# Kernel tuning notes

Hardware: AMD Instinct MI355X
Metric: run time of the kernel (lower is better)

## Reference

```python
import jax, jax.numpy as jnp
import numpy as np

B, H, L, D = 2, 16, 2048, 128

def setup_inputs() -> dict:
    key = jax.random.key(0)
    kq, kk, kv = jax.random.split(key, 3)
    Q = jax.random.normal(kq, (B, H, L, D), dtype=jnp.float32)
    K = jax.random.normal(kk, (B, H, L, D), dtype=jnp.float32)
    V = jax.random.normal(kv, (B, H, L, D), dtype=jnp.float32)
    # causal mask: True where attention is allowed
    mask = jnp.broadcast_to(jnp.tril(jnp.ones((L, L), dtype=bool)), (B, H, L, L))
    return {"Q": Q, "K": K, "V": V, "mask": mask}

def reference(Q, K, V, mask):
    d_k = Q.shape[-1]
    scale = 1.0 / jnp.sqrt(jnp.asarray(d_k, dtype=Q.dtype))
    # [B,H,Lq,Lk] score matrix (naive materialization, as in the original)
    scores = jnp.einsum('bhqd,bhkd->bhqk', Q, K) * scale
    scores = jnp.where(mask, scores, -jnp.inf)
    attn = jax.nn.softmax(scores, axis=-1)
    return jnp.einsum('bhqk,bhkd->bhqd', attn, V)
```

## Files before the change

kernel.cpp:

```cpp
#include <hip/hip_runtime.h>
#include <hip/hip_bf16.h>

namespace {

constexpr int Bc = 2, Hc = 16, Lc = 2048, Dc = 128;
constexpr int KVBLK = 64;
constexpr int BH  = Bc * Hc;
constexpr int NKT = Lc / KVBLK;
constexpr int QB  = 128;
constexpr int NQT = Lc / QB;
constexpr float SCALE = 0.08838834764831845f * 1.4426950408889634f;

using f32x4   = __attribute__((ext_vector_type(4))) float;
using f32x16  = __attribute__((ext_vector_type(16))) float;
using short8  = __attribute__((ext_vector_type(8))) short;

union FragU { short8 v; short4 h[2]; };
union PFU  { short8 v; unsigned u[4]; };

__device__ inline short f2bf(float f) {
  unsigned u = __builtin_bit_cast(unsigned, f);
  u += 0x7fffu + ((u >> 16) & 1u);
  return (short)(u >> 16);
}

__device__ inline void gload_lds16(const short* g, short* l) {
  __builtin_amdgcn_global_load_lds(
      (const __attribute__((address_space(1))) void*)g,
      (__attribute__((address_space(3))) void*)l, 16, 0, 0);
}

__global__ __launch_bounds__(256) void conv_kv(const float* __restrict__ Kg,
                                               const float* __restrict__ Vg,
                                               short* __restrict__ Kw,
                                               short* __restrict__ Vw) {
  __shared__ short Vs[64 * 130];
  const int b = blockIdx.x;
  if (b < 4096) {
    int tid = b * 256 + threadIdx.x;
    int x   = tid & 15;
    int row = (tid >> 4) & 63;
    int tb  = tid >> 10;
    int g   = x ^ (row & 7);
    int chunk = g >> 1, hi = g & 1;
    const float* src = Kg + ((size_t)tb * 64 + row) * 128 + chunk * 16 + hi * 4;
    float4 a = *(const float4*)src;
    float4 c = *(const float4*)(src + 8);
    short8 v;
    v[0] = f2bf(a.x); v[1] = f2bf(a.y); v[2] = f2bf(a.z); v[3] = f2bf(a.w);
    v[4] = f2bf(c.x); v[5] = f2bf(c.y); v[6] = f2bf(c.z); v[7] = f2bf(c.w);
    *(short8*)(Kw + (size_t)tb * 8192 + row * 128 + x * 8) = v;
  } else {
    int tb  = b - 4096;
    int tid = threadIdx.x;
    const float* vt = Vg + (size_t)tb * 8192;
#pragma unroll
    for (int p = 0; p < 8; ++p) {
      int g  = p * 256 + tid;
      int kv = g >> 5;
      int c4 = g & 31;
      float4 v = *((const float4*)vt + g);
      short* d = &Vs[kv * 130 + c4 * 4];
      d[0] = f2bf(v.x); d[1] = f2bf(v.y); d[2] = f2bf(v.z); d[3] = f2bf(v.w);
    }
    __syncthreads();
#pragma unroll
    for (int p = 0; p < 4; ++p) {
      int gg = p * 256 + tid;
      int d  = gg >> 3;
      int x  = gg & 7;
      int g  = x ^ (d & 7);
      int chunk = g >> 1, hi = g & 1;
      int k0 = chunk * 16 + hi * 4;
      short8 o;
#pragma unroll
      for (int j = 0; j < 4; ++j) o[j]     = Vs[(k0 + j)     * 130 + d];
#pragma unroll
      for (int j = 0; j < 4; ++j) o[4 + j] = Vs[(k0 + 8 + j) * 130 + d];
      *(short8*)(Vw + (size_t)tb * 8192 + d * 64 + x * 8) = o;
    }
  }
}

__global__ __launch_bounds__(256, 2) void attn_fwd5(
    const float* __restrict__ Qg, const short* __restrict__ Kw,
    const short* __restrict__ Vw, float* __restrict__ Og) {

  __shared__ __align__(16) short K2[2][8192];
  __shared__ __align__(16) short V3[3][8192];

  const int tid  = threadIdx.x;
  const int wave = tid >> 6;
  const int lane = tid & 63;
  const int hi   = lane >> 5;
  const int ln   = lane & 31;
  const int sw   = (ln & 7) << 4;

  const int bid = blockIdx.x;
  const int bh  = bid & (BH - 1);
  const int r5  = bid >> 5;
  const int qt  = (bid < 256) ? (NQT - 1 - r5) : (r5 - 8);
  const int q0w = qt * QB + wave * 32;

  const float* Qp  = Qg + (size_t)bh * Lc * Dc;
  float*       Op  = Og + (size_t)bh * Lc * Dc;
  const short* Kwp = Kw + (size_t)bh * NKT * 8192;
  const short* Vwp = Vw + (size_t)bh * NKT * 8192;

  short8 qf[8];
  {
    const float* qrow = Qp + (size_t)(q0w + ln) * Dc + hi * 4;
#pragma unroll
    for (int ks = 0; ks < 8; ++ks) {
      float4 a = *(const float4*)(qrow + ks * 16);
      float4 b = *(const float4*)(qrow + ks * 16 + 8);
      short8 v;
      v[0] = f2bf(a.x * SCALE); v[1] = f2bf(a.y * SCALE);
      v[2] = f2bf(a.z * SCALE); v[3] = f2bf(a.w * SCALE);
      v[4] = f2bf(b.x * SCALE); v[5] = f2bf(b.y * SCALE);
      v[6] = f2bf(b.z * SCALE); v[7] = f2bf(b.w * SCALE);
      qf[ks] = v;
    }
  }

  float m_run = -1e30f, l_run = 0.0f;
  f32x16 oacc[4];
#pragma unroll
  for (int nt = 0; nt < 4; ++nt)
#pragma unroll
    for (int r = 0; r < 16; ++r) oacc[nt][r] = 0.0f;

  const int ntiles = 2 * (qt + 1);
  const int tlast  = min(ntiles - 1, (q0w + 31) >> 6);

  auto stage = [&](int t, int kb, int vb) {
    const short* gk = Kwp + (size_t)t * 8192 + tid * 8;
    const short* gv = Vwp + (size_t)t * 8192 + tid * 8;
    short* lk = &K2[kb][tid * 8];
    short* lv = &V3[vb][tid * 8];
#pragma unroll
    for (int i = 0; i < 4; ++i) gload_lds16(gk + i * 2048, lk + i * 2048);
#pragma unroll
    for (int i = 0; i < 4; ++i) gload_lds16(gv + i * 2048, lv + i * 2048);
  };

  stage(0, 0, 0);
  int vb_prev = 2, vb_cur = 0, vb_next = 1;
  PFU pf[4];

  for (int t = 0; t < ntiles; ++t) {
    const int cur = t & 1;
    __builtin_amdgcn_s_barrier();
    if (t + 1 < ntiles) {
      stage(t + 1, cur ^ 1, vb_next);
      asm volatile("s_waitcnt vmcnt(8)" ::: "memory");
    } else {
      asm volatile("s_waitcnt vmcnt(0)" ::: "memory");
    }
    __builtin_amdgcn_s_barrier();
    __builtin_amdgcn_sched_barrier(0);

    const bool do_t = (t <= tlast);
    const bool do_pv = (t >= 1) && (t - 1 <= tlast);
    const int kv0 = t * KVBLK;

    f32x16 s0, s1;
    if (do_t) {
      const char* Kl = (const char*)&K2[cur][0];
#pragma unroll
      for (int r = 0; r < 16; ++r) { s0[r] = 0.0f; s1[r] = 0.0f; }
      __builtin_amdgcn_s_setprio(1);
#pragma unroll
      for (int ks = 0; ks < 8; ++ks) {
        FragU a0, a1;
        int col = (ks * 32 + hi * 16) ^ sw;
        a0.v = *(const short8*)(Kl + ln * 256        + col);
        a1.v = *(const short8*)(Kl + (32 + ln) * 256 + col);
        s0 = __builtin_amdgcn_mfma_f32_32x32x16_bf16(a0.v, qf[ks], s0, 0, 0, 0);
        s1 = __builtin_amdgcn_mfma_f32_32x32x16_bf16(a1.v, qf[ks], s1, 0, 0, 0);
      }
      __builtin_amdgcn_s_setprio(0);
    }

    if (do_pv) {
      const char* Vl = (const char*)&V3[vb_prev][0];
      __builtin_amdgcn_s_setprio(1);
#pragma unroll
      for (int nt = 0; nt < 4; ++nt) {
        const char* vrow = Vl + (nt * 32 + ln) * 128;
#pragma unroll
        for (int kc = 0; kc < 4; ++kc) {
          FragU b;
          b.v = *(const short8*)(vrow + ((kc * 32 + hi * 16) ^ sw));
          oacc[nt] = __builtin_amdgcn_mfma_f32_32x32x16_bf16(pf[kc].v, b.v, oacc[nt], 0, 0, 0);
        }
      }
      __builtin_amdgcn_s_setprio(0);
    }

    if (do_t) {
      if (kv0 + 63 > q0w) {
        const int qg = q0w + ln;
#pragma unroll
        for (int r = 0; r < 16; ++r) {
          int kvr = kv0 + (r & 3) + 8 * (r >> 2) + 4 * hi;
          if (kvr > qg)      s0[r] = -1e30f;
          if (kvr + 32 > qg) s1[r] = -1e30f;
        }
      }
      float ma = s0[0], mb = s0[8], mc = s1[0], md = s1[8];
#pragma unroll
      for (int r = 1; r < 8; ++r) {
        ma = fmaxf(ma, s0[r]); mb = fmaxf(mb, s0[8 + r]);
        mc = fmaxf(mc, s1[r]); md = fmaxf(md, s1[8 + r]);
      }
      float mx = fmaxf(fmaxf(ma, mb), fmaxf(mc, md));
      mx = fmaxf(mx, __shfl_xor(mx, 32));

      if (!__all(mx - m_run <= 8.0f)) {
        float mnew = fmaxf(m_run, mx);
        float corr = exp2f(m_run - mnew);
        m_run = mnew;
        l_run *= corr;
#pragma unroll
        for (int r = 0; r < 16; ++r) {
          int qrow = (r & 3) + 8 * (r >> 2) + 4 * hi;
          float c = __shfl(corr, qrow);
#pragma unroll
          for (int nt = 0; nt < 4; ++nt) oacc[nt][r] *= c;
        }
      }

      float rsp[4] = {0.f, 0.f, 0.f, 0.f};
#pragma unroll
      for (int kc = 0; kc < 4; ++kc) {
#pragma unroll
        for (int w = 0; w < 4; ++w) {
          int e = kc * 8 + w * 2;
          float v0 = (kc < 2) ? (float)s0[e]     : (float)s1[e - 16];
          float v1 = (kc < 2) ? (float)s0[e + 1] : (float)s1[e - 15];
          float e0 = exp2f(v0 - m_run);
          float e1 = exp2f(v1 - m_run);
          rsp[w] += e0 + e1;
          asm("v_cvt_pk_bf16_f32 %0, %1, %2" : "=v"(pf[kc].u[w]) : "v"(e0), "v"(e1));
        }
      }
      float rs = (rsp[0] + rsp[1]) + (rsp[2] + rsp[3]);
      rs += __shfl_xor(rs, 32);
      l_run += rs;
    }

    int tmp = vb_prev; vb_prev = vb_cur; vb_cur = vb_next; vb_next = tmp;
  }

  if (tlast == ntiles - 1) {
    const char* Vl = (const char*)&V3[vb_prev][0];
#pragma unroll
    for (int nt = 0; nt < 4; ++nt) {
      const char* vrow = Vl + (nt * 32 + ln) * 128;
#pragma unroll
      for (int kc = 0; kc < 4; ++kc) {
        FragU b;
        b.v = *(const short8*)(vrow + ((kc * 32 + hi * 16) ^ sw));
        oacc[nt] = __builtin_amdgcn_mfma_f32_32x32x16_bf16(pf[kc].v, b.v, oacc[nt], 0, 0, 0);
      }
    }
  }

  float linv = 1.0f / l_run;
#pragma unroll
  for (int r = 0; r < 16; ++r) {
    int qrow = (r & 3) + 8 * (r >> 2) + 4 * hi;
    float il = __shfl(linv, qrow);
    float* orow = Op + (size_t)(q0w + qrow) * Dc + ln;
#pragma unroll
    for (int nt = 0; nt < 4; ++nt)
      orow[nt * 32] = oacc[nt][r] * il;
  }
}

__device__ inline unsigned packbf(float a, float b) {
  return (unsigned)(unsigned short)f2bf(a) | ((unsigned)(unsigned short)f2bf(b) << 16);
}

__global__ __launch_bounds__(256, 2) void attn_fb(
    const float* __restrict__ Qg, const float* __restrict__ Kg,
    const float* __restrict__ Vg, float* __restrict__ Og) {
  __shared__ __align__(16) short Klds[KVBLK * Dc];
  __shared__ __align__(16) short Vt[Dc * 68];
  const int tid = threadIdx.x, wave = tid >> 6, lane = tid & 63;
  const int lg = lane >> 4, lr = lane & 15;
  const int bid = blockIdx.x;
  const int bh = bid & (BH - 1);
  const int qt = 31 - (bid >> 5);
  const int q0w = qt * 64 + wave * 16;
  const float* Qp = Qg + (size_t)bh * Lc * Dc;
  const float* Kp = Kg + (size_t)bh * Lc * Dc;
  const float* Vp = Vg + (size_t)bh * Lc * Dc;
  float* Op = Og + (size_t)bh * Lc * Dc;
  short8 qf[4];
  {
    const float* qrow = Qp + (size_t)(q0w + lr) * Dc;
#pragma unroll
    for (int dc = 0; dc < 4; ++dc) {
      float4 a = *(const float4*)(qrow + dc * 32 + lg * 4);
      float4 b = *(const float4*)(qrow + dc * 32 + 16 + lg * 4);
      short8 v;
      v[0]=f2bf(a.x*SCALE); v[1]=f2bf(a.y*SCALE); v[2]=f2bf(a.z*SCALE); v[3]=f2bf(a.w*SCALE);
      v[4]=f2bf(b.x*SCALE); v[5]=f2bf(b.y*SCALE); v[6]=f2bf(b.z*SCALE); v[7]=f2bf(b.w*SCALE);
      qf[dc] = v;
    }
  }
  const f32x4 zero4 = {0.f,0.f,0.f,0.f};
  float m_run = -1e30f, l_run = 0.0f;
  f32x4 oacc[8];
#pragma unroll
  for (int dt = 0; dt < 8; ++dt) oacc[dt] = zero4;
  const int ntiles = qt + 1, c4 = tid & 31, rK = tid >> 5;
  for (int t = 0; t < ntiles; ++t) {
    const int kv0 = t * KVBLK;
    __syncthreads();
#pragma unroll
    for (int p = 0; p < 8; ++p) {
      int row = rK + p * 8;
      float4 k4 = *(const float4*)(Kp + (size_t)(kv0 + row) * Dc + c4 * 4);
      short4 pk; pk.x=f2bf(k4.x); pk.y=f2bf(k4.y); pk.z=f2bf(k4.z); pk.w=f2bf(k4.w);
      *(short4*)((char*)Klds + row * 256 + ((c4 * 8) ^ ((row & 7) << 4))) = pk;
    }
#pragma unroll
    for (int p = 0; p < 4; ++p) {
      int r0 = rK * 2 + p * 16;
      float4 v0 = *(const float4*)(Vp + (size_t)(kv0 + r0) * Dc + c4 * 4);
      float4 v1 = *(const float4*)(Vp + (size_t)(kv0 + r0 + 1) * Dc + c4 * 4);
      char* vb = (char*)Vt + r0 * 2;
      *(unsigned*)(vb + (c4*4+0)*136) = packbf(v0.x, v1.x);
      *(unsigned*)(vb + (c4*4+1)*136) = packbf(v0.y, v1.y);
      *(unsigned*)(vb + (c4*4+2)*136) = packbf(v0.z, v1.z);
      *(unsigned*)(vb + (c4*4+3)*136) = packbf(v0.w, v1.w);
    }
    __syncthreads();
    f32x4 st[4];
#pragma unroll
    for (int mt = 0; mt < 4; ++mt) st[mt] = zero4;
#pragma unroll
    for (int dc = 0; dc < 4; ++dc)
#pragma unroll
      for (int mt = 0; mt < 4; ++mt) {
        int row = mt * 16 + lr, sw2 = (row & 7) << 4;
        FragU a;
        a.h[0] = *(short4*)((char*)Klds + row*256 + ((dc*64      + lg*8) ^ sw2));
        a.h[1] = *(short4*)((char*)Klds + row*256 + ((dc*64 + 32 + lg*8) ^ sw2));
        st[mt] = __builtin_amdgcn_mfma_f32_16x16x32_bf16(a.v, qf[dc], st[mt], 0, 0, 0);
      }
    if (t == ntiles - 1) {
      const int qg = q0w + lr;
#pragma unroll
      for (int mt = 0; mt < 4; ++mt)
#pragma unroll
        for (int r = 0; r < 4; ++r)
          if (kv0 + mt * 16 + lg * 4 + r > qg) st[mt][r] = -1e30f;
    }
    float mx = st[0][0];
#pragma unroll
    for (int mt = 0; mt < 4; ++mt)
#pragma unroll
      for (int r = 0; r < 4; ++r) mx = fmaxf(mx, st[mt][r]);
    mx = fmaxf(mx, __shfl_xor(mx, 16));
    mx = fmaxf(mx, __shfl_xor(mx, 32));
    float mnew = fmaxf(m_run, mx);
    float corr = exp2f(m_run - mnew);
    m_run = mnew;
    float pr[4][4]; float rs = 0.0f;
#pragma unroll
    for (int mt = 0; mt < 4; ++mt)
#pragma unroll
      for (int r = 0; r < 4; ++r) { float e = exp2f(st[mt][r] - mnew); pr[mt][r] = e; rs += e; }
    rs += __shfl_xor(rs, 16);
    rs += __shfl_xor(rs, 32);
    l_run = l_run * corr + rs;
#pragma unroll
    for (int r = 0; r < 4; ++r) {
      float c = __shfl(corr, (lane & 48) + lg * 4 + r);
#pragma unroll
      for (int dt = 0; dt < 8; ++dt) oacc[dt][r] *= c;
    }
    short8 pf2[2];
#pragma unroll
    for (int c = 0; c < 2; ++c) {
      short8 v;
      v[0]=f2bf(pr[2*c][0]); v[1]=f2bf(pr[2*c][1]); v[2]=f2bf(pr[2*c][2]); v[3]=f2bf(pr[2*c][3]);
      v[4]=f2bf(pr[2*c+1][0]); v[5]=f2bf(pr[2*c+1][1]); v[6]=f2bf(pr[2*c+1][2]); v[7]=f2bf(pr[2*c+1][3]);
      pf2[c] = v;
    }
#pragma unroll
    for (int dt = 0; dt < 8; ++dt) {
      int rowb = (dt * 16 + lr) * 136;
#pragma unroll
      for (int c = 0; c < 2; ++c) {
        FragU b;
        b.h[0] = *(short4*)((char*)Vt + rowb + c*64      + lg*8);
        b.h[1] = *(short4*)((char*)Vt + rowb + c*64 + 32 + lg*8);
        oacc[dt] = __builtin_amdgcn_mfma_f32_16x16x32_bf16(pf2[c], b.v, oacc[dt], 0, 0, 0);
      }
    }
  }
#pragma unroll
  for (int r = 0; r < 4; ++r) {
    float li = __shfl(l_run, (lane & 48) + lg * 4 + r);
    float inv = 1.0f / li;
    float* orow = Op + (size_t)(q0w + lg * 4 + r) * Dc;
#pragma unroll
    for (int dt = 0; dt < 8; ++dt) orow[dt * 16 + lr] = oacc[dt][r] * inv;
  }
}

}

extern "C" void kernel_launch(void* const* d_in, const int* in_sizes, int n_in,
                              void* d_out, int out_size, void* d_ws, size_t ws_size,
                              hipStream_t stream) {
  const float* Q = (const float*)d_in[0];
  const float* K = (const float*)d_in[1];
  const float* V = (const float*)d_in[2];
  float* O = (float*)d_out;
  const size_t elems = (size_t)BH * Lc * Dc;
  const size_t need  = 2 * elems * sizeof(short);
  if (ws_size >= need) {
    short* Kw = (short*)d_ws;
    short* Vw = Kw + elems;
    conv_kv<<<dim3(4096 + 1024), dim3(256), 0, stream>>>(K, V, Kw, Vw);
    attn_fwd5<<<dim3(BH * NQT), dim3(256), 0, stream>>>(Q, Kw, Vw, O);
  } else {
    attn_fb<<<dim3(BH * NKT), dim3(256), 0, stream>>>(Q, K, V, O);
  }
}
```

Baseline: 95.11 us.

## Load K/V MFMA fragments directly from global into registers, drop LDS staging

The K/V pre-conversion kernel now writes bf16 data in exact per-lane MFMA fragment order, so the attention kernel can load K and V fragments straight from global memory into registers instead of staging tiles through double/triple-buffered LDS with barriers. The main loop is restructured to compute QK^T, softmax and PV within the same iteration, prefetching the next tile's fragments into registers. This removes LDS traffic and block-wide barriers, and each wave now iterates only over its own causal range. In exchange, every wave independently reads the full K/V tiles from global/L2, with no sharing across the 4 waves. The 32 extra fragment registers also raise register pressure, and the cross-iteration software pipelining of PV behind the next QK is lost.

```diff
diff --git a/kernel.cpp b/kernel.cpp
--- a/kernel.cpp
+++ b/kernel.cpp
@@ -16,18 +16,11 @@
 using short8  = __attribute__((ext_vector_type(8))) short;
 
 union FragU { short8 v; short4 h[2]; };
-union PFU  { short8 v; unsigned u[4]; };
 
 __device__ inline short f2bf(float f) {
   unsigned u = __builtin_bit_cast(unsigned, f);
   u += 0x7fffu + ((u >> 16) & 1u);
   return (short)(u >> 16);
-}
-
-__device__ inline void gload_lds16(const short* g, short* l) {
-  __builtin_amdgcn_global_load_lds(
-      (const __attribute__((address_space(1))) void*)g,
-      (__attribute__((address_space(3))) void*)l, 16, 0, 0);
 }
 
 __global__ __launch_bounds__(256) void conv_kv(const float* __restrict__ Kg,
@@ -37,19 +30,20 @@
   __shared__ short Vs[64 * 130];
   const int b = blockIdx.x;
   if (b < 4096) {
-    int tid = b * 256 + threadIdx.x;
-    int x   = tid & 15;
-    int row = (tid >> 4) & 63;
-    int tb  = tid >> 10;
-    int g   = x ^ (row & 7);
-    int chunk = g >> 1, hi = g & 1;
-    const float* src = Kg + ((size_t)tb * 64 + row) * 128 + chunk * 16 + hi * 4;
+    int tid  = b * 256 + threadIdx.x;
+    int rem  = tid & 1023;
+    int tb   = tid >> 10;
+    int ks   = rem >> 7;
+    int s    = (rem >> 6) & 1;
+    int lane = rem & 63;
+    int hi   = lane >> 5, ln = lane & 31;
+    const float* src = Kg + ((size_t)tb * 64 + s * 32 + ln) * 128 + ks * 16 + hi * 4;
     float4 a = *(const float4*)src;
     float4 c = *(const float4*)(src + 8);
     short8 v;
     v[0] = f2bf(a.x); v[1] = f2bf(a.y); v[2] = f2bf(a.z); v[3] = f2bf(a.w);
     v[4] = f2bf(c.x); v[5] = f2bf(c.y); v[6] = f2bf(c.z); v[7] = f2bf(c.w);
-    *(short8*)(Kw + (size_t)tb * 8192 + row * 128 + x * 8) = v;
+    *(short8*)(Kw + (size_t)tb * 8192 + rem * 8) = v;
   } else {
     int tb  = b - 4096;
     int tid = threadIdx.x;
@@ -66,35 +60,32 @@
     __syncthreads();
 #pragma unroll
     for (int p = 0; p < 4; ++p) {
-      int gg = p * 256 + tid;
-      int d  = gg >> 3;
-      int x  = gg & 7;
-      int g  = x ^ (d & 7);
-      int chunk = g >> 1, hi = g & 1;
-      int k0 = chunk * 16 + hi * 4;
+      int g    = p * 256 + tid;
+      int nt   = g >> 8;
+      int kc   = (g >> 6) & 3;
+      int lane = g & 63;
+      int hi   = lane >> 5, ln = lane & 31;
+      int d    = nt * 32 + ln;
+      int k0   = kc * 16 + hi * 4;
       short8 o;
 #pragma unroll
       for (int j = 0; j < 4; ++j) o[j]     = Vs[(k0 + j)     * 130 + d];
 #pragma unroll
       for (int j = 0; j < 4; ++j) o[4 + j] = Vs[(k0 + 8 + j) * 130 + d];
-      *(short8*)(Vw + (size_t)tb * 8192 + d * 64 + x * 8) = o;
-    }
-  }
-}
-
-__global__ __launch_bounds__(256, 2) void attn_fwd5(
+      *(short8*)(Vw + (size_t)tb * 8192 + g * 8) = o;
+    }
+  }
+}
+
+__global__ __launch_bounds__(256, 2) void attn_fwd6(
     const float* __restrict__ Qg, const short* __restrict__ Kw,
     const short* __restrict__ Vw, float* __restrict__ Og) {
-
-  __shared__ __align__(16) short K2[2][8192];
-  __shared__ __align__(16) short V3[3][8192];
 
   const int tid  = threadIdx.x;
   const int wave = tid >> 6;
   const int lane = tid & 63;
   const int hi   = lane >> 5;
   const int ln   = lane & 31;
-  const int sw   = (ln & 7) << 4;
 
   const int bid = blockIdx.x;
   const int bh  = bid & (BH - 1);
@@ -104,8 +95,8 @@
 
   const float* Qp  = Qg + (size_t)bh * Lc * Dc;
   float*       Op  = Og + (size_t)bh * Lc * Dc;
-  const short* Kwp = Kw + (size_t)bh * NKT * 8192;
-  const short* Vwp = Vw + (size_t)bh * NKT * 8192;
+  const short* kb  = Kw + (size_t)bh * NKT * 8192 + lane * 8;
+  const short* vb  = Vw + (size_t)bh * NKT * 8192 + lane * 8;
 
   short8 qf[8];
   {
@@ -130,140 +121,99 @@
 #pragma unroll
     for (int r = 0; r < 16; ++r) oacc[nt][r] = 0.0f;
 
-  const int ntiles = 2 * (qt + 1);
-  const int tlast  = min(ntiles - 1, (q0w + 31) >> 6);
-
-  auto stage = [&](int t, int kb, int vb) {
-    const short* gk = Kwp + (size_t)t * 8192 + tid * 8;
-    const short* gv = Vwp + (size_t)t * 8192 + tid * 8;
-    short* lk = &K2[kb][tid * 8];
-    short* lv = &V3[vb][tid * 8];
-#pragma unroll
-    for (int i = 0; i < 4; ++i) gload_lds16(gk + i * 2048, lk + i * 2048);
-#pragma unroll
-    for (int i = 0; i < 4; ++i) gload_lds16(gv + i * 2048, lv + i * 2048);
-  };
-
-  stage(0, 0, 0);
-  int vb_prev = 2, vb_cur = 0, vb_next = 1;
-  PFU pf[4];
-
-  for (int t = 0; t < ntiles; ++t) {
-    const int cur = t & 1;
-    __builtin_amdgcn_s_barrier();
-    if (t + 1 < ntiles) {
-      stage(t + 1, cur ^ 1, vb_next);
-      asm volatile("s_waitcnt vmcnt(8)" ::: "memory");
-    } else {
-      asm volatile("s_waitcnt vmcnt(0)" ::: "memory");
-    }
-    __builtin_amdgcn_s_barrier();
-    __builtin_amdgcn_sched_barrier(0);
-
-    const bool do_t = (t <= tlast);
-    const bool do_pv = (t >= 1) && (t - 1 <= tlast);
+  const int tl = (q0w + 31) >> 6;
+
+  FragU kf[16], vf[16];
+#pragma unroll
+  for (int i = 0; i < 16; ++i) kf[i].v = *(const short8*)(kb + i * 512);
+#pragma unroll
+  for (int i = 0; i < 16; ++i) vf[i].v = *(const short8*)(vb + i * 512);
+
+  for (int t = 0; t <= tl; ++t) {
+    f32x16 s0, s1;
+#pragma unroll
+    for (int r = 0; r < 16; ++r) { s0[r] = 0.0f; s1[r] = 0.0f; }
+    __builtin_amdgcn_s_setprio(1);
+#pragma unroll
+    for (int ks = 0; ks < 8; ++ks) {
+      s0 = __builtin_amdgcn_mfma_f32_32x32x16_bf16(kf[ks * 2 + 0].v, qf[ks], s0, 0, 0, 0);
+      s1 = __builtin_amdgcn_mfma_f32_32x32x16_bf16(kf[ks * 2 + 1].v, qf[ks], s1, 0, 0, 0);
+    }
+    __builtin_amdgcn_s_setprio(0);
+
+    if (t < tl) {
+      const short* kn = kb + (size_t)(t + 1) * 8192;
+#pragma unroll
+      for (int i = 0; i < 16; ++i) kf[i].v = *(const short8*)(kn + i * 512);
+    }
+
     const int kv0 = t * KVBLK;
-
-    f32x16 s0, s1;
-    if (do_t) {
-      const char* Kl = (const char*)&K2[cur][0];
-#pragma unroll
-      for (int r = 0; r < 16; ++r) { s0[r] = 0.0f; s1[r] = 0.0f; }
-      __builtin_amdgcn_s_setprio(1);
-#pragma unroll
-      for (int ks = 0; ks < 8; ++ks) {
-        FragU a0, a1;
-        int col = (ks * 32 + hi * 16) ^ sw;
-        a0.v = *(const short8*)(Kl + ln * 256        + col);
-        a1.v = *(const short8*)(Kl + (32 + ln) * 256 + col);
-        s0 = __builtin_amdgcn_mfma_f32_32x32x16_bf16(a0.v, qf[ks], s0, 0, 0, 0);
-        s1 = __builtin_amdgcn_mfma_f32_32x32x16_bf16(a1.v, qf[ks], s1, 0, 0, 0);
-      }
-      __builtin_amdgcn_s_setprio(0);
-    }
-
-    if (do_pv) {
-      const char* Vl = (const char*)&V3[vb_prev][0];
-      __builtin_amdgcn_s_setprio(1);
-#pragma unroll
-      for (int nt = 0; nt < 4; ++nt) {
-        const char* vrow = Vl + (nt * 32 + ln) * 128;
-#pragma unroll
-        for (int kc = 0; kc < 4; ++kc) {
-          FragU b;
-          b.v = *(const short8*)(vrow + ((kc * 32 + hi * 16) ^ sw));
-          oacc[nt] = __builtin_amdgcn_mfma_f32_32x32x16_bf16(pf[kc].v, b.v, oacc[nt], 0, 0, 0);
-        }
-      }
-      __builtin_amdgcn_s_setprio(0);
-    }
-
-    if (do_t) {
-      if (kv0 + 63 > q0w) {
-        const int qg = q0w + ln;
-#pragma unroll
-        for (int r = 0; r < 16; ++r) {
-          int kvr = kv0 + (r & 3) + 8 * (r >> 2) + 4 * hi;
-          if (kvr > qg)      s0[r] = -1e30f;
-          if (kvr + 32 > qg) s1[r] = -1e30f;
-        }
-      }
-      float ma = s0[0], mb = s0[8], mc = s1[0], md = s1[8];
-#pragma unroll
-      for (int r = 1; r < 8; ++r) {
-        ma = fmaxf(ma, s0[r]); mb = fmaxf(mb, s0[8 + r]);
-        mc = fmaxf(mc, s1[r]); md = fmaxf(md, s1[8 + r]);
-      }
-      float mx = fmaxf(fmaxf(ma, mb), fmaxf(mc, md));
-      mx = fmaxf(mx, __shfl_xor(mx, 32));
-
-      if (!__all(mx - m_run <= 8.0f)) {
-        float mnew = fmaxf(m_run, mx);
-        float corr = exp2f(m_run - mnew);
-        m_run = mnew;
-        l_run *= corr;
-#pragma unroll
-        for (int r = 0; r < 16; ++r) {
-          int qrow = (r & 3) + 8 * (r >> 2) + 4 * hi;
-          float c = __shfl(corr, qrow);
-#pragma unroll
-          for (int nt = 0; nt < 4; ++nt) oacc[nt][r] *= c;
-        }
-      }
-
-      float rsp[4] = {0.f, 0.f, 0.f, 0.f};
+    if (kv0 + 63 > q0w) {
+      const int qg = q0w + ln;
+#pragma unroll
+      for (int r = 0; r < 16; ++r) {
+        int kvr = kv0 + (r & 3) + 8 * (r >> 2) + 4 * hi;
+        if (kvr > qg)      s0[r] = -1e30f;
+        if (kvr + 32 > qg) s1[r] = -1e30f;
+      }
+    }
+
+    float ma = s0[0], mb = s0[8], mc = s1[0], md = s1[8];
+#pragma unroll
+    for (int r = 1; r < 8; ++r) {
+      ma = fmaxf(ma, s0[r]); mb = fmaxf(mb, s0[8 + r]);
+      mc = fmaxf(mc, s1[r]); md = fmaxf(md, s1[8 + r]);
+    }
+    float mx = fmaxf(fmaxf(ma, mb), fmaxf(mc, md));
+    mx = fmaxf(mx, __shfl_xor(mx, 32));
+
+    if (!__all(mx - m_run <= 8.0f)) {
+      float mnew = fmaxf(m_run, mx);
+      float corr = exp2f(m_run - mnew);
+      m_run = mnew;
+      l_run *= corr;
+#pragma unroll
+      for (int r = 0; r < 16; ++r) {
+        int qrow = (r & 3) + 8 * (r >> 2) + 4 * hi;
+        float c = __shfl(corr, qrow);
+#pragma unroll
+        for (int nt = 0; nt < 4; ++nt) oacc[nt][r] *= c;
+      }
+    }
+
+    float rsp[4] = {0.f, 0.f, 0.f, 0.f};
+    short8 pf[4];
+#pragma unroll
+    for (int kc = 0; kc < 4; ++kc) {
+      short8 v;
+#pragma unroll
+      for (int e = 0; e < 8; ++e) {
+        float sv = (kc < 2) ? s0[kc * 8 + e] : s1[(kc - 2) * 8 + e];
+        float p = exp2f(sv - m_run);
+        rsp[e & 3] += p;
+        v[e] = f2bf(p);
+      }
+      pf[kc] = v;
+    }
+    float rs = (rsp[0] + rsp[1]) + (rsp[2] + rsp[3]);
+    rs += __shfl_xor(rs, 32);
+    l_run += rs;
+
+    __builtin_amdgcn_s_setprio(1);
+#pragma unroll
+    for (int nt = 0; nt < 4; ++nt) {
 #pragma unroll
       for (int kc = 0; kc < 4; ++kc) {
-#pragma unroll
-        for (int w = 0; w < 4; ++w) {
-          int e = kc * 8 + w * 2;
-          float v0 = (kc < 2) ? (float)s0[e]     : (float)s1[e - 16];
-          float v1 = (kc < 2) ? (float)s0[e + 1] : (float)s1[e - 15];
-          float e0 = exp2f(v0 - m_run);
-          float e1 = exp2f(v1 - m_run);
-          rsp[w] += e0 + e1;
-          asm("v_cvt_pk_bf16_f32 %0, %1, %2" : "=v"(pf[kc].u[w]) : "v"(e0), "v"(e1));
-        }
-      }
-      float rs = (rsp[0] + rsp[1]) + (rsp[2] + rsp[3]);
-      rs += __shfl_xor(rs, 32);
-      l_run += rs;
-    }
-
-    int tmp = vb_prev; vb_prev = vb_cur; vb_cur = vb_next; vb_next = tmp;
-  }
-
-  if (tlast == ntiles - 1) {
-    const char* Vl = (const char*)&V3[vb_prev][0];
-#pragma unroll
-    for (int nt = 0; nt < 4; ++nt) {
-      const char* vrow = Vl + (nt * 32 + ln) * 128;
-#pragma unroll
-      for (int kc = 0; kc < 4; ++kc) {
-        FragU b;
-        b.v = *(const short8*)(vrow + ((kc * 32 + hi * 16) ^ sw));
-        oacc[nt] = __builtin_amdgcn_mfma_f32_32x32x16_bf16(pf[kc].v, b.v, oacc[nt], 0, 0, 0);
-      }
+        oacc[nt] = __builtin_amdgcn_mfma_f32_32x32x16_bf16(
+            pf[kc], vf[nt * 4 + kc].v, oacc[nt], 0, 0, 0);
+      }
+    }
+    __builtin_amdgcn_s_setprio(0);
+
+    if (t < tl) {
+      const short* vn = vb + (size_t)(t + 1) * 8192;
+#pragma unroll
+      for (int i = 0; i < 16; ++i) vf[i].v = *(const short8*)(vn + i * 512);
     }
   }
 
@@ -332,11 +282,11 @@
       int r0 = rK * 2 + p * 16;
       float4 v0 = *(const float4*)(Vp + (size_t)(kv0 + r0) * Dc + c4 * 4);
       float4 v1 = *(const float4*)(Vp + (size_t)(kv0 + r0 + 1) * Dc + c4 * 4);
-      char* vb = (char*)Vt + r0 * 2;
-      *(unsigned*)(vb + (c4*4+0)*136) = packbf(v0.x, v1.x);
-      *(unsigned*)(vb + (c4*4+1)*136) = packbf(v0.y, v1.y);
-      *(unsigned*)(vb + (c4*4+2)*136) = packbf(v0.z, v1.z);
-      *(unsigned*)(vb + (c4*4+3)*136) = packbf(v0.w, v1.w);
+      char* vb2 = (char*)Vt + r0 * 2;
+      *(unsigned*)(vb2 + (c4*4+0)*136) = packbf(v0.x, v1.x);
+      *(unsigned*)(vb2 + (c4*4+1)*136) = packbf(v0.y, v1.y);
+      *(unsigned*)(vb2 + (c4*4+2)*136) = packbf(v0.z, v1.z);
+      *(unsigned*)(vb2 + (c4*4+3)*136) = packbf(v0.w, v1.w);
     }
     __syncthreads();
     f32x4 st[4];
@@ -429,7 +379,7 @@
     short* Kw = (short*)d_ws;
     short* Vw = Kw + elems;
     conv_kv<<<dim3(4096 + 1024), dim3(256), 0, stream>>>(K, V, Kw, Vw);
-    attn_fwd5<<<dim3(BH * NQT), dim3(256), 0, stream>>>(Q, Kw, Vw, O);
+    attn_fwd6<<<dim3(BH * NQT), dim3(256), 0, stream>>>(Q, Kw, Vw, O);
   } else {
     attn_fb<<<dim3(BH * NKT), dim3(256), 0, stream>>>(Q, K, V, O);
   }
```

New measurement: 153.8 us. 1.62x slower.
